# Optimization experiments

Measured on AMD Instinct MI355X. Metric: run time of the kernel, lower is better.

## Reference

```python
import jax, jax.numpy as jnp
import numpy as np

N = 50000      # num atoms
E = 800000     # num edges
F = 64         # atom_fea_len
NBR = 64       # nbr_fea_len
NCONV = 3
T = 4096       # pooled target atoms
STATE = 2
VOCAB = 100
EPS = 1e-5


def setup_inputs() -> dict:
    key = jax.random.key(0)
    ks = jax.random.split(key, 20)
    Z = 2 * F + NBR  # concat message width
    inp = {
        "x_types": jax.random.randint(ks[0], (N,), 0, VOCAB),
        "edge_index": jax.random.randint(ks[1], (2, E), 0, N),
        "edge_attr": jax.random.normal(ks[2], (E, NBR), dtype=jnp.float32),
        "target": jax.random.randint(ks[3], (T,), 0, N),
        "emb": jax.random.normal(ks[4], (VOCAB, F), dtype=jnp.float32),
        "Wc": jax.random.normal(ks[5], (NCONV, F, Z), dtype=jnp.float32) * 0.05,
        "bc": jnp.zeros((NCONV, F), jnp.float32),
        "Wf": jax.random.normal(ks[6], (NCONV, 1, Z), dtype=jnp.float32) * 0.05,
        "bf": jnp.zeros((NCONV, 1), jnp.float32),
        "g1": jnp.ones((NCONV, F), jnp.float32),
        "b1": jnp.zeros((NCONV, F), jnp.float32),
        "g2": jnp.ones((NCONV, F), jnp.float32),
        "b2": jnp.zeros((NCONV, F), jnp.float32),
        "Wfc": jax.random.normal(ks[7], (F, F), dtype=jnp.float32) * 0.05,
        "bfc": jnp.zeros((F,), jnp.float32),
        "Ws": jax.random.normal(ks[8], (STATE, F), dtype=jnp.float32) * 0.05,
        "bs": jnp.zeros((STATE,), jnp.float32),
    }
    return inp


def _segment_softmax(logits, idx, n):
    # per-target-node softmax over variable-size edge neighborhoods
    m = jax.ops.segment_max(logits, idx, num_segments=n)
    m = jnp.where(jnp.isfinite(m), m, 0.0)
    e = jnp.exp(logits - m[idx])
    s = jax.ops.segment_sum(e, idx, num_segments=n)
    return e / (s[idx] + 1e-16)


def _batchnorm(x, gamma, beta):
    # training-mode BatchNorm1d: biased batch stats over dim 0
    mu = x.mean(0)
    var = x.var(0)
    return (x - mu) * jax.lax.rsqrt(var + EPS) * gamma + beta


def reference(x_types, edge_index, edge_attr, target, emb, Wc, bc, Wf, bf,
              g1, b1, g2, b2, Wfc, bfc, Ws, bs):
    x = emb[x_types]                      # [N, F]
    # flow='target_to_source': i = edge_index[0] (aggregate here), j = edge_index[1]
    idx_i = edge_index[0]
    idx_j = edge_index[1]
    ones = jnp.ones((edge_index.shape[1],), x.dtype)
    cnt = jax.ops.segment_sum(ones, idx_i, num_segments=x.shape[0])
    denom = jnp.maximum(cnt, 1.0)[:, None]
    for l in range(NCONV):
        z = jnp.concatenate([x[idx_i], x[idx_j], edge_attr], axis=1)  # [E, 2F+NBR]
        core = jax.nn.relu(_batchnorm(z @ Wc[l].T + bc[l], g1[l], b1[l]))  # [E, F]
        filt = (z @ Wf[l].T + bf[l])[:, 0]                                  # [E]
        alpha = _segment_softmax(filt, idx_i, x.shape[0])[:, None]          # [E, 1]
        agg = jax.ops.segment_sum(alpha * core, idx_i, num_segments=x.shape[0]) / denom
        x = jax.nn.relu(_batchnorm(agg, g2[l], b2[l]) + x)
    h = jax.nn.relu(x[target])            # [T, F]
    h = jax.nn.relu(h @ Wfc.T + bfc)
    logits = h @ Ws.T + bs                # [T, STATE]
    return jax.nn.softmax(logits, axis=-1)
```

## Files before the change

### kernel.cpp

```cpp
#include <hip/hip_runtime.h>
#include <math.h>

#define N_ATOMS 50000
#define N_EDGES 800000
#define F 64
#define Z 192
#define NCONV 3
#define T_TGT 4096
#define EPS 1e-5f
#define SLOTS 64
#define NB_SCAN 196
#define NBLK_E 1250
#define STEPS_E 10
#define NGRP_N 3125
#define NBLK_N 782

typedef __attribute__((ext_vector_type(4))) float f32x4;
typedef __attribute__((ext_vector_type(8))) short s16x8;
typedef __attribute__((ext_vector_type(8))) __bf16 bf16x8;

static __device__ __forceinline__ float bf2f(unsigned short u) {
    return __uint_as_float(((unsigned int)u) << 16);
}
static __device__ __forceinline__ unsigned short f2bf(float f) {
    unsigned int u = __float_as_uint(f);
    unsigned int r = u + 0x7FFFu + ((u >> 16) & 1u);
    return (unsigned short)(r >> 16);
}
static __device__ __forceinline__ bf16x8 pack8(float4 a, float4 b) {
    s16x8 r;
    r[0] = (short)f2bf(a.x); r[1] = (short)f2bf(a.y);
    r[2] = (short)f2bf(a.z); r[3] = (short)f2bf(a.w);
    r[4] = (short)f2bf(b.x); r[5] = (short)f2bf(b.y);
    r[6] = (short)f2bf(b.z); r[7] = (short)f2bf(b.w);
    return __builtin_bit_cast(bf16x8, r);
}
static __device__ __forceinline__ uint2 pack4(float a, float b, float c, float d) {
    uint2 r;
    r.x = (unsigned int)f2bf(a) | ((unsigned int)f2bf(b) << 16);
    r.y = (unsigned int)f2bf(c) | ((unsigned int)f2bf(d) << 16);
    return r;
}


__global__ void k_embed(const int* __restrict__ types, const float* __restrict__ emb,
                        float* __restrict__ x, unsigned short* __restrict__ xb) {
    int idx = blockIdx.x * 256 + threadIdx.x;
    if (idx < N_ATOMS * F) {
        int n = idx >> 6, f = idx & 63;
        float v = emb[types[n] * F + f];
        x[idx] = v;
        xb[idx] = f2bf(v);
    }
}

__global__ void k_degree(const int* __restrict__ idx_i, int* __restrict__ cnt) {
    int e = blockIdx.x * 256 + threadIdx.x;
    if (e < N_EDGES) atomicAdd(&cnt[idx_i[e]], 1);
}

__global__ void k_scanA(const int* __restrict__ cnt, int* __restrict__ bsum) {
    __shared__ int s[256];
    int base = blockIdx.x * 256, t = threadIdx.x;
    s[t] = (base + t < N_ATOMS) ? cnt[base + t] : 0;
    __syncthreads();
    for (int o = 128; o > 0; o >>= 1) {
        if (t < o) s[t] += s[t + o];
        __syncthreads();
    }
    if (t == 0) bsum[blockIdx.x] = s[0];
}

__global__ void k_scanB(int* __restrict__ bsum, int* __restrict__ rowptr) {
    __shared__ int s[256];
    int t = threadIdx.x;
    int v = (t < NB_SCAN) ? bsum[t] : 0;
    s[t] = v;
    __syncthreads();
    for (int o = 1; o < 256; o <<= 1) {
        int add = (t >= o) ? s[t - o] : 0;
        __syncthreads();
        s[t] += add;
        __syncthreads();
    }
    if (t < NB_SCAN) bsum[t] = s[t] - v;
    if (t == 0) rowptr[N_ATOMS] = N_EDGES;
}

__global__ void k_scanC(const int* __restrict__ cnt, const int* __restrict__ bsum,
                        int* __restrict__ rowptr) {
    __shared__ int s[256];
    int base = blockIdx.x * 256, t = threadIdx.x;
    int v = (base + t < N_ATOMS) ? cnt[base + t] : 0;
    s[t] = v;
    __syncthreads();
    for (int o = 1; o < 256; o <<= 1) {
        int add = (t >= o) ? s[t - o] : 0;
        __syncthreads();
        s[t] += add;
        __syncthreads();
    }
    if (base + t < N_ATOMS) rowptr[base + t] = bsum[blockIdx.x] + s[t] - v;
}

__global__ void k_scatter(const int* __restrict__ idx_i, const int* __restrict__ idx_j,
                          const int* __restrict__ rowptr, int* __restrict__ wofs,
                          int* __restrict__ i_s, int* __restrict__ j_s,
                          int* __restrict__ einv) {
    int e = blockIdx.x * 256 + threadIdx.x;
    if (e < N_EDGES) {
        int i = idx_i[e];
        int pos = rowptr[i] + atomicAdd(&wofs[i], 1);
        i_s[pos] = i;
        j_s[pos] = idx_j[e];
        einv[e] = pos;
    }
}

__global__ void k_prep(const float* __restrict__ ea, const int* __restrict__ einv,
                       const float* __restrict__ Wf,
                       unsigned short* __restrict__ eab, float* __restrict__ pe) {
    int row = blockIdx.x * 256 + threadIdx.x;
    if (row >= N_EDGES) return;
    int pos = einv[row];
    const float* src = ea + (size_t)row * F;
    unsigned short* dst = eab + (size_t)pos * F;
    float d0 = 0.f, d1 = 0.f, d2 = 0.f;
    #pragma unroll
    for (int ch = 0; ch < 8; ++ch) {
        float4 a = *(const float4*)(src + ch * 8);
        float4 b = *(const float4*)(src + ch * 8 + 4);
        float vv[8] = {a.x, a.y, a.z, a.w, b.x, b.y, b.z, b.w};
        #pragma unroll
        for (int j = 0; j < 8; ++j) {
            int k = 128 + ch * 8 + j;
            d0 += vv[j] * Wf[k];
            d1 += vv[j] * Wf[Z + k];
            d2 += vv[j] * Wf[2 * Z + k];
        }
        *(bf16x8*)(dst + ch * 8) = pack8(a, b);
    }
    pe[pos] = d0;
    pe[N_EDGES + pos] = d1;
    pe[2 * N_EDGES + pos] = d2;
}

__global__ __launch_bounds__(256) void k_node_mm(
    const unsigned short* __restrict__ xb,
    const float* __restrict__ Wc, const float* __restrict__ Wf,
    float* __restrict__ u, unsigned short* __restrict__ v,
    float* __restrict__ pi, float* __restrict__ pj)
{
    __shared__ unsigned short WL[18 * 64 * 8];
    int t = threadIdx.x;
    int lane = t & 63, w = t >> 6;
    int c = lane & 15, g = lane >> 4;
    int goff = g * 8;

    #pragma unroll
    for (int rep = 0; rep < 5; ++rep) {
        int f = rep * 4 + w;
        if (f < 18) {
            int kt = f / 9, m = f % 9;
            bf16x8 val;
            if (m < 8) {
                int colbase = (m < 4) ? 0 : 64;
                const float* wp = Wc + (size_t)((m & 3) * 16 + c) * Z + colbase + kt * 32 + goff;
                val = pack8(*(const float4*)wp, *(const float4*)(wp + 4));
            } else {
                s16x8 zz = {0, 0, 0, 0, 0, 0, 0, 0};
                val = __builtin_bit_cast(bf16x8, zz);
                if (c == 0) {
                    const float* wp = Wf + kt * 32 + goff;
                    val = pack8(*(const float4*)wp, *(const float4*)(wp + 4));
                } else if (c == 1) {
                    const float* wp = Wf + 64 + kt * 32 + goff;
                    val = pack8(*(const float4*)wp, *(const float4*)(wp + 4));
                }
            }
            *(bf16x8*)(WL + ((size_t)f * 64 + lane) * 8) = val;
        }
    }
    __syncthreads();

    int grp = blockIdx.x * 4 + w;
    if (grp >= NGRP_N) return;
    int node = grp * 16 + c;
    const unsigned short* xr = xb + (size_t)node * F;
    bf16x8 X0 = *(const bf16x8*)(xr + goff);
    bf16x8 X1 = *(const bf16x8*)(xr + 32 + goff);

    #define LFR(f) (*(const bf16x8*)(WL + ((size_t)(f) * 64 + lane) * 8))
    f32x4 au[4], av[4], ap = (f32x4){0.f, 0.f, 0.f, 0.f};
    #pragma unroll
    for (int m = 0; m < 4; ++m) {
        au[m] = (f32x4){0.f, 0.f, 0.f, 0.f};
        av[m] = (f32x4){0.f, 0.f, 0.f, 0.f};
        au[m] = __builtin_amdgcn_mfma_f32_16x16x32_bf16(LFR(m), X0, au[m], 0, 0, 0);
        au[m] = __builtin_amdgcn_mfma_f32_16x16x32_bf16(LFR(9 + m), X1, au[m], 0, 0, 0);
        av[m] = __builtin_amdgcn_mfma_f32_16x16x32_bf16(LFR(4 + m), X0, av[m], 0, 0, 0);
        av[m] = __builtin_amdgcn_mfma_f32_16x16x32_bf16(LFR(13 + m), X1, av[m], 0, 0, 0);
    }
    ap = __builtin_amdgcn_mfma_f32_16x16x32_bf16(LFR(8), X0, ap, 0, 0, 0);
    ap = __builtin_amdgcn_mfma_f32_16x16x32_bf16(LFR(17), X1, ap, 0, 0, 0);
    #undef LFR

    float* urow = u + (size_t)node * F + g * 4;
    unsigned short* vrow = v + (size_t)node * F + g * 4;
    #pragma unroll
    for (int m = 0; m < 4; ++m) {
        *(f32x4*)(urow + m * 16) = au[m];
        *(uint2*)(vrow + m * 16) = pack4(av[m][0], av[m][1], av[m][2], av[m][3]);
    }
    if (g == 0) {
        pi[node] = ap[0];
        pj[node] = ap[1];
    }
}

__global__ __launch_bounds__(256, 3) void k_edge2(
    const unsigned short* __restrict__ eab,
    const float* __restrict__ u, const unsigned short* __restrict__ v,
    const int* __restrict__ i_s, const int* __restrict__ j_s,
    const float* __restrict__ Wc,
    const float* __restrict__ pe, const float* __restrict__ pi, const float* __restrict__ pj,
    unsigned short* __restrict__ y, float* __restrict__ filt,
    float* __restrict__ stats)
{
    __shared__ unsigned short WL[8 * 64 * 8];
    int t = threadIdx.x;
    int lane = t & 63, w = t >> 6;
    int c = lane & 15, g = lane >> 4;
    int goff = g * 8;

    #pragma unroll
    for (int rep = 0; rep < 2; ++rep) {
        int f = w * 2 + rep;
        int kt = f >> 2, nt = f & 3;
        const float* wp = Wc + (size_t)(nt * 16 + c) * Z + 128 + kt * 32 + goff;
        *(bf16x8*)(WL + ((size_t)f * 64 + lane) * 8) =
            pack8(*(const float4*)wp, *(const float4*)(wp + 4));
    }
    __syncthreads();

    bf16x8 A[2][4];
    #pragma unroll
    for (int kt = 0; kt < 2; ++kt)
        #pragma unroll
        for (int nt = 0; nt < 4; ++nt)
            A[kt][nt] = *(const bf16x8*)(WL + ((size_t)(kt * 4 + nt) * 64 + lane) * 8);

    float ssum[4][4] = {{0.f}}, ssq[4][4] = {{0.f}};

    int e = blockIdx.x * (STEPS_E * 64) + w * 16 + c;
    int ie = i_s[e], je = j_s[e];
    bf16x8 E0 = *(const bf16x8*)(eab + (size_t)e * F + goff);
    bf16x8 E1 = *(const bf16x8*)(eab + (size_t)e * F + 32 + goff);

    for (int s = 0; s < STEPS_E; ++s) {
        const float* ur = u + (size_t)ie * F + g * 4;
        const unsigned short* vr = v + (size_t)je * F + g * 4;
        float4 uu[4];
        uint2 vv[4];
        #pragma unroll
        for (int nt = 0; nt < 4; ++nt) {
            uu[nt] = *(const float4*)(ur + nt * 16);
            vv[nt] = *(const uint2*)(vr + nt * 16);
        }
        float fe = 0.f, fi = 0.f, fj = 0.f;
        if (g == 0) { fe = pe[e]; fi = pi[ie]; fj = pj[je]; }

        int e2 = e, ie2 = ie, je2 = je;
        bf16x8 E0n = E0, E1n = E1;
        if (s + 1 < STEPS_E) {
            e2 = e + 64;
            ie2 = i_s[e2];
            je2 = j_s[e2];
            E0n = *(const bf16x8*)(eab + (size_t)e2 * F + goff);
            E1n = *(const bf16x8*)(eab + (size_t)e2 * F + 32 + goff);
        }

        f32x4 acc[4];
        #pragma unroll
        for (int nt = 0; nt < 4; ++nt) {
            acc[nt] = (f32x4){0.f, 0.f, 0.f, 0.f};
            acc[nt] = __builtin_amdgcn_mfma_f32_16x16x32_bf16(A[0][nt], E0, acc[nt], 0, 0, 0);
            acc[nt] = __builtin_amdgcn_mfma_f32_16x16x32_bf16(A[1][nt], E1, acc[nt], 0, 0, 0);
        }

        unsigned short* yr = y + (size_t)e * F + g * 4;
        #pragma unroll
        for (int nt = 0; nt < 4; ++nt) {
            float y0 = acc[nt][0] + uu[nt].x + bf2f((unsigned short)(vv[nt].x & 0xffff));
            float y1 = acc[nt][1] + uu[nt].y + bf2f((unsigned short)(vv[nt].x >> 16));
            float y2 = acc[nt][2] + uu[nt].z + bf2f((unsigned short)(vv[nt].y & 0xffff));
            float y3 = acc[nt][3] + uu[nt].w + bf2f((unsigned short)(vv[nt].y >> 16));
            ssum[nt][0] += y0; ssq[nt][0] += y0 * y0;
            ssum[nt][1] += y1; ssq[nt][1] += y1 * y1;
            ssum[nt][2] += y2; ssq[nt][2] += y2 * y2;
            ssum[nt][3] += y3; ssq[nt][3] += y3 * y3;
            *(uint2*)(yr + nt * 16) = pack4(y0, y1, y2, y3);
        }
        if (g == 0) filt[e] = fe + fi + fj;

        e = e2; ie = ie2; je = je2; E0 = E0n; E1 = E1n;
    }

    int slot = (blockIdx.x & (SLOTS - 1)) * 128;
    #pragma unroll
    for (int nt = 0; nt < 4; ++nt) {
        #pragma unroll
        for (int q = 0; q < 4; ++q) {
            float S = ssum[nt][q], Q = ssq[nt][q];
            S += __shfl_xor(S, 1, 64); S += __shfl_xor(S, 2, 64);
            S += __shfl_xor(S, 4, 64); S += __shfl_xor(S, 8, 64);
            Q += __shfl_xor(Q, 1, 64); Q += __shfl_xor(Q, 2, 64);
            Q += __shfl_xor(Q, 4, 64); Q += __shfl_xor(Q, 8, 64);
            if (c == 0) {
                int f = nt * 16 + g * 4 + q;
                atomicAdd(&stats[slot + f], S);
                atomicAdd(&stats[slot + 64 + f], Q);
            }
        }
    }
}


__global__ void k_finbn(const float* __restrict__ stats, float* __restrict__ bnp, float count) {
    int f = threadIdx.x;
    float S = 0.f, Q = 0.f;
    for (int s = 0; s < SLOTS; ++s) {
        S += stats[s * 128 + f];
        Q += stats[s * 128 + 64 + f];
    }
    float mu = S / count;
    float var = Q / count - mu * mu;
    var = fmaxf(var, 0.f);
    bnp[f] = mu;
    bnp[64 + f] = 1.f / sqrtf(var + EPS);
}

__global__ __launch_bounds__(256) void k_node_agg(
    const unsigned short* __restrict__ y, const float* __restrict__ filt,
    const int* __restrict__ rowptr, const int* __restrict__ cnt,
    const float* __restrict__ bnp, const float* __restrict__ g1, const float* __restrict__ b1,
    float* __restrict__ agg)
{
    int t = threadIdx.x;
    int lane = t & 63;
    int node = blockIdx.x * 4 + (t >> 6);
    int beg = rowptr[node], end = rowptr[node + 1];
    int es = lane >> 4, fq = lane & 15;
    float4 mu4 = *(const float4*)(bnp + fq * 4);
    float4 rs4 = *(const float4*)(bnp + 64 + fq * 4);
    float4 ga4 = *(const float4*)(g1 + fq * 4);
    float4 be4 = *(const float4*)(b1 + fq * 4);

    float fm = -INFINITY;
    for (int i = beg + lane; i < end; i += 64) fm = fmaxf(fm, filt[i]);
    #pragma unroll
    for (int o = 32; o > 0; o >>= 1) fm = fmaxf(fm, __shfl_xor(fm, o, 64));

    float a0 = 0.f, a1 = 0.f, a2 = 0.f, a3 = 0.f, ss = 0.f;
    for (int base = beg; base < end; base += 4) {
        int ee = base + es;
        int eec = min(ee, end - 1);
        float wgt = (ee < end) ? expf(filt[eec] - fm) : 0.f;
        ushort4 yv = *(const ushort4*)(y + (size_t)eec * F + fq * 4);
        float c0 = fmaxf((bf2f(yv.x) - mu4.x) * rs4.x * ga4.x + be4.x, 0.f);
        float c1 = fmaxf((bf2f(yv.y) - mu4.y) * rs4.y * ga4.y + be4.y, 0.f);
        float c2 = fmaxf((bf2f(yv.z) - mu4.z) * rs4.z * ga4.z + be4.z, 0.f);
        float c3 = fmaxf((bf2f(yv.w) - mu4.w) * rs4.w * ga4.w + be4.w, 0.f);
        a0 += wgt * c0; a1 += wgt * c1; a2 += wgt * c2; a3 += wgt * c3;
        ss += wgt;
    }
    #pragma unroll
    for (int o = 16; o <= 32; o <<= 1) {
        a0 += __shfl_xor(a0, o, 64);
        a1 += __shfl_xor(a1, o, 64);
        a2 += __shfl_xor(a2, o, 64);
        a3 += __shfl_xor(a3, o, 64);
        ss += __shfl_xor(ss, o, 64);
    }
    if (lane < 16) {
        float dn = fmaxf((float)cnt[node], 1.f);
        float inv = 1.f / ((ss + 1e-16f) * dn);
        float4 o4;
        o4.x = a0 * inv; o4.y = a1 * inv; o4.z = a2 * inv; o4.w = a3 * inv;
        *(float4*)(agg + (size_t)node * F + fq * 4) = o4;
    }
}

__global__ void k_colstats(const float* __restrict__ agg, float* __restrict__ stats) {
    __shared__ float buf[4][64];
    int t = threadIdx.x;
    int f = t & 63, g = t >> 6;
    float S = 0.f, Q = 0.f;
    for (int n = blockIdx.x * 4 + g; n < N_ATOMS; n += gridDim.x * 4) {
        float v = agg[(size_t)n * F + f];
        S += v; Q += v * v;
    }
    buf[g][f] = S;
    __syncthreads();
    if (t < 64) {
        float s2 = buf[0][t] + buf[1][t] + buf[2][t] + buf[3][t];
        atomicAdd(&stats[(blockIdx.x & 63) * 128 + t], s2);
    }
    __syncthreads();
    buf[g][f] = Q;
    __syncthreads();
    if (t < 64) {
        float q2 = buf[0][t] + buf[1][t] + buf[2][t] + buf[3][t];
        atomicAdd(&stats[(blockIdx.x & 63) * 128 + 64 + t], q2);
    }
}

__global__ void k_node_upd(const float* __restrict__ agg, const float* __restrict__ bnp,
                           const float* __restrict__ g2, const float* __restrict__ b2,
                           const float* __restrict__ xin, float* __restrict__ xout,
                           unsigned short* __restrict__ xbout) {
    int idx = blockIdx.x * 256 + threadIdx.x;
    if (idx < N_ATOMS * F) {
        int f = idx & 63;
        float v = (agg[idx] - bnp[f]) * bnp[64 + f] * g2[f] + b2[f] + xin[idx];
        v = fmaxf(v, 0.f);
        xout[idx] = v;
        xbout[idx] = f2bf(v);
    }
}


__global__ __launch_bounds__(256) void k_head(
    const float* __restrict__ x, const int* __restrict__ target,
    const float* __restrict__ Wfc, const float* __restrict__ bfc,
    const float* __restrict__ Ws, const float* __restrict__ bs,
    float* __restrict__ out)
{
    __shared__ float hbuf[4][64];
    int t = threadIdx.x;
    int lane = t & 63, w = t >> 6;
    int tt = blockIdx.x * 4 + w;
    int a = target[min(tt, T_TGT - 1)];
    float h = fmaxf(x[(size_t)a * F + lane], 0.f);
    hbuf[w][lane] = h;
    __syncthreads();
    float acc = bfc[lane];
    #pragma unroll 8
    for (int k = 0; k < F; ++k) acc += hbuf[w][k] * Wfc[lane * F + k];
    float h2 = fmaxf(acc, 0.f);
    float p0 = h2 * Ws[lane];
    float p1 = h2 * Ws[F + lane];
    #pragma unroll
    for (int o = 32; o > 0; o >>= 1) {
        p0 += __shfl_xor(p0, o, 64);
        p1 += __shfl_xor(p1, o, 64);
    }
    if (lane == 0 && tt < T_TGT) {
        float l0 = p0 + bs[0], l1 = p1 + bs[1];
        float mx = fmaxf(l0, l1);
        float e0v = expf(l0 - mx), e1v = expf(l1 - mx);
        float inv = 1.f / (e0v + e1v);
        out[tt * 2 + 0] = e0v * inv;
        out[tt * 2 + 1] = e1v * inv;
    }
}


extern "C" void kernel_launch(void* const* d_in, const int* in_sizes, int n_in,
                              void* d_out, int out_size, void* d_ws, size_t ws_size,
                              hipStream_t stream)
{
    const int*   x_types = (const int*)d_in[0];
    const int*   eidx    = (const int*)d_in[1];
    const float* ea      = (const float*)d_in[2];
    const int*   target  = (const int*)d_in[3];
    const float* emb     = (const float*)d_in[4];
    const float* Wc      = (const float*)d_in[5];
    const float* Wf      = (const float*)d_in[7];
    const float* g1      = (const float*)d_in[9];
    const float* b1      = (const float*)d_in[10];
    const float* g2      = (const float*)d_in[11];
    const float* b2      = (const float*)d_in[12];
    const float* Wfc     = (const float*)d_in[13];
    const float* bfc     = (const float*)d_in[14];
    const float* Ws      = (const float*)d_in[15];
    const float* bs      = (const float*)d_in[16];
    float* out = (float*)d_out;
    const int* idx_i = eidx;
    const int* idx_j = eidx + N_EDGES;

    char* p = (char*)d_ws;
    auto alloc = [&](size_t bytes) {
        char* r = p;
        p += (bytes + 255) & ~(size_t)255;
        return r;
    };
    float* xa            = (float*)alloc((size_t)N_ATOMS * F * 4);
    float* xb_f          = (float*)alloc((size_t)N_ATOMS * F * 4);
    unsigned short* x16a = (unsigned short*)alloc((size_t)N_ATOMS * F * 2);
    unsigned short* x16b = (unsigned short*)alloc((size_t)N_ATOMS * F * 2);
    unsigned short* eab  = (unsigned short*)alloc((size_t)N_EDGES * F * 2);
    unsigned short* ybuf = (unsigned short*)alloc((size_t)N_EDGES * F * 2);
    float* filt          = (float*)alloc((size_t)N_EDGES * 4);
    float* pe            = (float*)alloc((size_t)NCONV * N_EDGES * 4);
    float* ubuf          = (float*)alloc((size_t)N_ATOMS * F * 4);
    unsigned short* vbuf = (unsigned short*)alloc((size_t)N_ATOMS * F * 2);
    float* pi            = (float*)alloc((size_t)N_ATOMS * 4);
    float* pj            = (float*)alloc((size_t)N_ATOMS * 4);
    float* agg           = (float*)alloc((size_t)N_ATOMS * F * 4);
    int* cnt             = (int*)alloc((size_t)N_ATOMS * 4);
    int* rowptr          = (int*)alloc((size_t)(N_ATOMS + 1) * 4);
    int* wofs            = (int*)alloc((size_t)N_ATOMS * 4);
    int* i_s             = (int*)alloc((size_t)N_EDGES * 4);
    int* j_s             = (int*)alloc((size_t)N_EDGES * 4);
    int* einv            = (int*)alloc((size_t)N_EDGES * 4);
    int* bsum            = (int*)alloc(256 * 4);
    float* stats         = (float*)alloc(SLOTS * 128 * 4);
    float* bnp1          = (float*)alloc(128 * 4);
    float* bnp2          = (float*)alloc(128 * 4);
    (void)ws_size; (void)in_sizes; (void)n_in; (void)out_size;

    hipMemsetAsync(cnt, 0, (size_t)N_ATOMS * 4, stream);
    hipMemsetAsync(wofs, 0, (size_t)N_ATOMS * 4, stream);
    k_embed<<<(N_ATOMS * F + 255) / 256, 256, 0, stream>>>(x_types, emb, xa, x16a);
    k_degree<<<(N_EDGES + 255) / 256, 256, 0, stream>>>(idx_i, cnt);
    k_scanA<<<NB_SCAN, 256, 0, stream>>>(cnt, bsum);
    k_scanB<<<1, 256, 0, stream>>>(bsum, rowptr);
    k_scanC<<<NB_SCAN, 256, 0, stream>>>(cnt, bsum, rowptr);
    k_scatter<<<(N_EDGES + 255) / 256, 256, 0, stream>>>(idx_i, idx_j, rowptr, wofs,
                                                         i_s, j_s, einv);
    k_prep<<<N_EDGES / 256, 256, 0, stream>>>(ea, einv, Wf, eab, pe);

    float* xcur = xa;
    float* xnxt = xb_f;
    unsigned short* x16cur = x16a;
    unsigned short* x16nxt = x16b;
    for (int l = 0; l < NCONV; ++l) {
        k_node_mm<<<NBLK_N, 256, 0, stream>>>(x16cur,
            Wc + (size_t)l * F * Z, Wf + (size_t)l * Z, ubuf, vbuf, pi, pj);
        hipMemsetAsync(stats, 0, SLOTS * 128 * 4, stream);
        k_edge2<<<NBLK_E, 256, 0, stream>>>(
            eab, ubuf, vbuf, i_s, j_s,
            Wc + (size_t)l * F * Z,
            pe + (size_t)l * N_EDGES, pi, pj,
            ybuf, filt, stats);
        k_finbn<<<1, 64, 0, stream>>>(stats, bnp1, (float)N_EDGES);
        k_node_agg<<<N_ATOMS / 4, 256, 0, stream>>>(ybuf, filt, rowptr, cnt, bnp1,
                                                    g1 + (size_t)l * F, b1 + (size_t)l * F, agg);
        hipMemsetAsync(stats, 0, SLOTS * 128 * 4, stream);
        k_colstats<<<256, 256, 0, stream>>>(agg, stats);
        k_finbn<<<1, 64, 0, stream>>>(stats, bnp2, (float)N_ATOMS);
        k_node_upd<<<(N_ATOMS * F + 255) / 256, 256, 0, stream>>>(
            agg, bnp2, g2 + (size_t)l * F, b2 + (size_t)l * F, xcur, xnxt, x16nxt);
        float* tf = xcur; xcur = xnxt; xnxt = tf;
        unsigned short* ts = x16cur; x16cur = x16nxt; x16nxt = ts;
    }
    k_head<<<T_TGT / 4, 256, 0, stream>>>(xcur, target, Wfc, bfc, Ws, bs, out);
}
```

Measured before the change: 815.7 us.

## Fold edge filter projection into edge MFMA and parallelize edge-attr bf16 conversion

The per-edge filter dot product over edge attributes, which was precomputed for all three layers in the prep kernel and stored in a pe buffer, now runs inside the edge kernel as a fifth MFMA column tile (Wf row padded with zeros). The prep kernel only converts edge attributes to bf16, using eight threads per row for more parallel, coalesced access. This removes the scalar dot products in prep and the pe reads in each layer, at the cost of two extra MFMAs per edge step and more registers. The filter logit is now computed from bf16 inputs, which slightly lowers its precision.

```diff
diff --git a/kernel.cpp b/kernel.cpp
--- a/kernel.cpp
+++ b/kernel.cpp
@@ -117,32 +117,17 @@
     }
 }
 
-__global__ void k_prep(const float* __restrict__ ea, const int* __restrict__ einv,
-                       const float* __restrict__ Wf,
-                       unsigned short* __restrict__ eab, float* __restrict__ pe) {
-    int row = blockIdx.x * 256 + threadIdx.x;
+__global__ void k_prep2(const float* __restrict__ ea, const int* __restrict__ einv,
+                        unsigned short* __restrict__ eab) {
+    int idx = blockIdx.x * 256 + threadIdx.x;
+    int row = idx >> 3;
     if (row >= N_EDGES) return;
+    int seg = (idx & 7) * 8;
+    const float* src = ea + (size_t)row * F + seg;
+    float4 a = *(const float4*)src;
+    float4 b = *(const float4*)(src + 4);
     int pos = einv[row];
-    const float* src = ea + (size_t)row * F;
-    unsigned short* dst = eab + (size_t)pos * F;
-    float d0 = 0.f, d1 = 0.f, d2 = 0.f;
-    #pragma unroll
-    for (int ch = 0; ch < 8; ++ch) {
-        float4 a = *(const float4*)(src + ch * 8);
-        float4 b = *(const float4*)(src + ch * 8 + 4);
-        float vv[8] = {a.x, a.y, a.z, a.w, b.x, b.y, b.z, b.w};
-        #pragma unroll
-        for (int j = 0; j < 8; ++j) {
-            int k = 128 + ch * 8 + j;
-            d0 += vv[j] * Wf[k];
-            d1 += vv[j] * Wf[Z + k];
-            d2 += vv[j] * Wf[2 * Z + k];
-        }
-        *(bf16x8*)(dst + ch * 8) = pack8(a, b);
-    }
-    pe[pos] = d0;
-    pe[N_EDGES + pos] = d1;
-    pe[2 * N_EDGES + pos] = d2;
+    *(bf16x8*)(eab + (size_t)pos * F + seg) = pack8(a, b);
 }
 
 __global__ __launch_bounds__(256) void k_node_mm(
@@ -222,33 +207,45 @@
     const unsigned short* __restrict__ eab,
     const float* __restrict__ u, const unsigned short* __restrict__ v,
     const int* __restrict__ i_s, const int* __restrict__ j_s,
-    const float* __restrict__ Wc,
-    const float* __restrict__ pe, const float* __restrict__ pi, const float* __restrict__ pj,
+    const float* __restrict__ Wc, const float* __restrict__ Wf,
+    const float* __restrict__ pi, const float* __restrict__ pj,
     unsigned short* __restrict__ y, float* __restrict__ filt,
     float* __restrict__ stats)
 {
-    __shared__ unsigned short WL[8 * 64 * 8];
+    __shared__ unsigned short WL[10 * 64 * 8];
     int t = threadIdx.x;
     int lane = t & 63, w = t >> 6;
     int c = lane & 15, g = lane >> 4;
     int goff = g * 8;
 
     #pragma unroll
-    for (int rep = 0; rep < 2; ++rep) {
-        int f = w * 2 + rep;
-        int kt = f >> 2, nt = f & 3;
-        const float* wp = Wc + (size_t)(nt * 16 + c) * Z + 128 + kt * 32 + goff;
-        *(bf16x8*)(WL + ((size_t)f * 64 + lane) * 8) =
-            pack8(*(const float4*)wp, *(const float4*)(wp + 4));
-    }
-    __syncthreads();
-
-    bf16x8 A[2][4];
+    for (int rep = 0; rep < 3; ++rep) {
+        int f = rep * 4 + w;
+        if (f < 10) {
+            int kt = f / 5, nt = f % 5;
+            bf16x8 val;
+            if (nt < 4) {
+                const float* wp = Wc + (size_t)(nt * 16 + c) * Z + 128 + kt * 32 + goff;
+                val = pack8(*(const float4*)wp, *(const float4*)(wp + 4));
+            } else {
+                s16x8 zz = {0, 0, 0, 0, 0, 0, 0, 0};
+                val = __builtin_bit_cast(bf16x8, zz);
+                if (c == 0) {
+                    const float* wp = Wf + 128 + kt * 32 + goff;
+                    val = pack8(*(const float4*)wp, *(const float4*)(wp + 4));
+                }
+            }
+            *(bf16x8*)(WL + ((size_t)f * 64 + lane) * 8) = val;
+        }
+    }
+    __syncthreads();
+
+    bf16x8 A[2][5];
     #pragma unroll
     for (int kt = 0; kt < 2; ++kt)
         #pragma unroll
-        for (int nt = 0; nt < 4; ++nt)
-            A[kt][nt] = *(const bf16x8*)(WL + ((size_t)(kt * 4 + nt) * 64 + lane) * 8);
+        for (int nt = 0; nt < 5; ++nt)
+            A[kt][nt] = *(const bf16x8*)(WL + ((size_t)(kt * 5 + nt) * 64 + lane) * 8);
 
     float ssum[4][4] = {{0.f}}, ssq[4][4] = {{0.f}};
 
@@ -267,8 +264,8 @@
             uu[nt] = *(const float4*)(ur + nt * 16);
             vv[nt] = *(const uint2*)(vr + nt * 16);
         }
-        float fe = 0.f, fi = 0.f, fj = 0.f;
-        if (g == 0) { fe = pe[e]; fi = pi[ie]; fj = pj[je]; }
+        float fi = 0.f, fj = 0.f;
+        if (g == 0) { fi = pi[ie]; fj = pj[je]; }
 
         int e2 = e, ie2 = ie, je2 = je;
         bf16x8 E0n = E0, E1n = E1;
@@ -280,9 +277,9 @@
             E1n = *(const bf16x8*)(eab + (size_t)e2 * F + 32 + goff);
         }
 
-        f32x4 acc[4];
+        f32x4 acc[5];
         #pragma unroll
-        for (int nt = 0; nt < 4; ++nt) {
+        for (int nt = 0; nt < 5; ++nt) {
             acc[nt] = (f32x4){0.f, 0.f, 0.f, 0.f};
             acc[nt] = __builtin_amdgcn_mfma_f32_16x16x32_bf16(A[0][nt], E0, acc[nt], 0, 0, 0);
             acc[nt] = __builtin_amdgcn_mfma_f32_16x16x32_bf16(A[1][nt], E1, acc[nt], 0, 0, 0);
@@ -301,7 +298,7 @@
             ssum[nt][3] += y3; ssq[nt][3] += y3 * y3;
             *(uint2*)(yr + nt * 16) = pack4(y0, y1, y2, y3);
         }
-        if (g == 0) filt[e] = fe + fi + fj;
+        if (g == 0) filt[e] = acc[4][0] + fi + fj;
 
         e = e2; ie = ie2; je = je2; E0 = E0n; E1 = E1n;
     }
@@ -502,7 +499,6 @@
     unsigned short* eab  = (unsigned short*)alloc((size_t)N_EDGES * F * 2);
     unsigned short* ybuf = (unsigned short*)alloc((size_t)N_EDGES * F * 2);
     float* filt          = (float*)alloc((size_t)N_EDGES * 4);
-    float* pe            = (float*)alloc((size_t)NCONV * N_EDGES * 4);
     float* ubuf          = (float*)alloc((size_t)N_ATOMS * F * 4);
     unsigned short* vbuf = (unsigned short*)alloc((size_t)N_ATOMS * F * 2);
     float* pi            = (float*)alloc((size_t)N_ATOMS * 4);
@@ -529,7 +525,7 @@
     k_scanC<<<NB_SCAN, 256, 0, stream>>>(cnt, bsum, rowptr);
     k_scatter<<<(N_EDGES + 255) / 256, 256, 0, stream>>>(idx_i, idx_j, rowptr, wofs,
                                                          i_s, j_s, einv);
-    k_prep<<<N_EDGES / 256, 256, 0, stream>>>(ea, einv, Wf, eab, pe);
+    k_prep2<<<(N_EDGES * 8) / 256, 256, 0, stream>>>(ea, einv, eab);
 
     float* xcur = xa;
     float* xnxt = xb_f;
@@ -541,8 +537,8 @@
         hipMemsetAsync(stats, 0, SLOTS * 128 * 4, stream);
         k_edge2<<<NBLK_E, 256, 0, stream>>>(
             eab, ubuf, vbuf, i_s, j_s,
-            Wc + (size_t)l * F * Z,
-            pe + (size_t)l * N_EDGES, pi, pj,
+            Wc + (size_t)l * F * Z, Wf + (size_t)l * Z,
+            pi, pj,
             ybuf, filt, stats);
         k_finbn<<<1, 64, 0, stream>>>(stats, bnp1, (float)N_EDGES);
         k_node_agg<<<N_ATOMS / 4, 256, 0, stream>>>(ybuf, filt, rowptr, cnt, bnp1,
```

Result: faster. 724.0 us (-11.2%).
